# Kernel optimization log

Measured on AMD Instinct MI355X. Metric: run time of the kernel, lower is better.

Reference implementation:

```python
import jax, jax.numpy as jnp
import numpy as np

C = 256
K = 9
PAD = (K - 1) // 2  # 4


def setup_inputs() -> dict:
    key = jax.random.key(0)
    k1, k2, k3 = jax.random.split(key, 3)
    fea = jax.random.normal(k1, (8, C, 128, 128), dtype=jnp.float32)
    # Conv2d(C, C, (1,9)) with kernel height 1 -> 1D conv weight [O, I, K]
    fan_in = C * K
    bound = 1.0 / np.sqrt(fan_in)
    weight = jax.random.uniform(k2, (C, C, K), dtype=jnp.float32, minval=-bound, maxval=bound)
    bias = jax.random.uniform(k3, (C,), dtype=jnp.float32, minval=-bound, maxval=bound)
    return {"fea": fea, "weight": weight, "bias": bias}


def _conv_relu(x, weight, bias):
    # x: [n, c, w] -> 1D conv along width, then ReLU (matches Conv2d (1,9) on a 1-row slice)
    y = jax.lax.conv_general_dilated(
        x, weight, window_strides=(1,), padding=[(PAD, PAD)],
        dimension_numbers=("NCW", "OIW", "NCW"))
    return jax.nn.relu(y + bias[None, :, None])


def reference(fea, weight, bias):
    n, c, h, w = fea.shape
    rows = jnp.moveaxis(fea, 2, 0)  # [h, n, c, w]

    def step(carry, row):
        new = _conv_relu(carry, weight, bias) + row
        return new, new

    # forward (top-down) scan: fea_stack[i] = conv(fea_stack[i-1]) + fea_stack[i]
    _, ys_f = jax.lax.scan(step, rows[0], rows[1:])
    full = jnp.concatenate([rows[:1], ys_f], axis=0)  # [h, n, c, w]

    # backward (bottom-up) scan over i = h-2 .. 1
    mid = full[1:h - 1]
    _, ys_b = jax.lax.scan(step, full[h - 1], mid[::-1])
    out_rows = jnp.concatenate([full[:1], ys_b[::-1], full[h - 1:]], axis=0)

    return jnp.moveaxis(out_rows, 0, 2)  # back to [n, c, h, w]
```

## Files before the change

### kernel.cpp

```cpp
#include <hip/hip_runtime.h>

typedef _Float16 f16;
typedef _Float16 f16x8 __attribute__((ext_vector_type(8)));
typedef _Float16 f16x4 __attribute__((ext_vector_type(4)));
typedef float    f32x16 __attribute__((ext_vector_type(16)));
typedef unsigned long long u64;

#define N_   8
#define C_   256
#define H_   128
#define W_   128
#define K_   9
#define PAD_ 4
#define WP_  136

#define WELEMS (8*9*16*64*8)
#define XT_SZ  (N_*WP_*256)
#define XBUF_F16 (N_*WP_*512)
#define NBLK   256
#define NSTEP  253

__device__ __host__ inline int xpos(int ci, int wp) {
    int g = ((ci >> 3) + 2 * wp) & 31;
    return g * 8 + (ci & 7);
}

__global__ __launch_bounds__(256) void prep_w(const float* __restrict__ w,
                                              f16* __restrict__ wh, f16* __restrict__ wl) {
    int t = blockIdx.x * 256 + threadIdx.x;
    if (t >= WELEMS) return;
    int j = t & 7;      int q = t >> 3;
    int lane = q & 63;  q >>= 6;
    int c = q & 15;     q >>= 4;
    int k = q % 9;      int ct = q / 9;
    int co = ct * 32 + (lane & 31);
    int ci = c * 16 + (lane >> 5) * 8 + j;
    float wf = w[(co * C_ + ci) * K_ + k];
    f16 hi = (f16)wf;
    f16 lo = (f16)(wf - (float)hi);
    wh[t] = hi;  wl[t] = lo;
}

__global__ __launch_bounds__(256) void prep_x0(const float* __restrict__ fea,
                                               f16* __restrict__ xb0, f16* __restrict__ xb1) {
    int t = blockIdx.x * 256 + threadIdx.x;
    if (t >= XT_SZ) return;
    int ci = t & 255;
    int wp = (t >> 8) % WP_;
    int n  = t / (WP_ * 256);
    int w  = wp - PAD_;
    bool pad = (unsigned)w >= (unsigned)W_;
    float v = pad ? 0.0f : fea[((size_t)(n * C_ + ci) * H_ + 0) * W_ + w];
    f16 hi = (f16)v;
    f16 lo = (f16)(v - (float)hi);
    size_t row = ((size_t)n * WP_ + wp) * 512;
    int p = xpos(ci, wp);
    xb0[row + p] = hi;  xb0[row + 256 + p] = lo;
    if (pad) { xb1[row + p] = (f16)0.f; xb1[row + 256 + p] = (f16)0.f; }
}

__global__ __launch_bounds__(256) void copy_row0(const float* __restrict__ fea,
                                                 float* __restrict__ out) {
    int idx = blockIdx.x * 256 + threadIdx.x;
    if (idx >= N_ * C_ * W_) return;
    int w = idx % W_;
    int nc = idx / W_;
    size_t off = (size_t)nc * (H_ * W_) + w;
    out[off] = fea[off];
}

__global__ __launch_bounds__(512, 2) void conv_persist(
    f16* __restrict__ xb0, f16* __restrict__ xb1,
    const f16* __restrict__ whp, const f16* __restrict__ wlp,
    const float* __restrict__ bias, const float* __restrict__ fea,
    float* out, unsigned* ctr)
{
    __shared__ unsigned char Xs[40 * 1024];
    float* red = (float*)Xs;

    const int b   = blockIdx.x;
    const int n   = b & 7;
    const int ct  = (b >> 3) & 7;
    const int wq  = b >> 6;
    const int w0  = wq * 32;
    const int tid = threadIdx.x;
    const int wv  = tid >> 6;
    const int l   = tid & 63;
    const int m   = l & 31;
    const int hh  = l >> 5;
    unsigned* flags = ctr + n * 64;
    const int bslot = b >> 3;

    f16x8 wkh[9][2], wkl[9][2];
    #pragma unroll
    for (int k = 0; k < 9; ++k)
        #pragma unroll
        for (int cs = 0; cs < 2; ++cs) {
            size_t o = ((((size_t)ct * 9 + k) * 16 + (wv * 2 + cs)) * 64 + l) * 8;
            wkh[k][cs] = *(const f16x8*)&whp[o];
            wkl[k][cs] = *(const f16x8*)&wlp[o];
        }

    f16* bufs[2] = {xb0, xb1};

    const int dq = wv & 3;
    const int co_base = ct * 32 + dq * 8 + hh * 4;
    const size_t HW = (size_t)H_ * W_;
    float4 bv = *(const float4*)&bias[co_base];
    const float bvr[4] = {bv.x, bv.y, bv.z, bv.w};

    for (int step = 0; step < NSTEP; ++step) {
        const int  cur   = step & 1;
        const bool fwd   = step < 127;
        const int  h_out = fwd ? (step + 1) : (NSTEP - step);
        const float* radd = fwd ? fea : out;
        const size_t obase = (((size_t)(n * C_ + co_base)) * H_ + h_out) * W_ + w0 + m;

        {
            const u64* src = (const u64*)(bufs[cur] + ((size_t)n * WP_ + w0) * 512);
            u64 v[10];
            #pragma unroll
            for (int ii = 0; ii < 10; ++ii)
                v[ii] = __hip_atomic_load(src + ii * 512 + tid,
                                          __ATOMIC_RELAXED, __HIP_MEMORY_SCOPE_AGENT);
            #pragma unroll
            for (int ii = 0; ii < 10; ++ii)
                *(u64*)(Xs + (size_t)(ii * 512 + tid) * 8) = v[ii];
        }
        float rv[4] = {0.f, 0.f, 0.f, 0.f};
        if (wv < 4) {
            #pragma unroll
            for (int c2 = 0; c2 < 4; ++c2)
                rv[c2] = radd[obase + (size_t)c2 * HW];
        }
        __syncthreads();

        f32x16 a0{}, cr{};
        #pragma unroll
        for (int k = 0; k < 9; ++k) {
            #pragma unroll
            for (int cs = 0; cs < 2; ++cs) {
                const int rl  = m + k;
                const int gsw = (((wv * 2 + cs) * 2 + hh + 2 * rl) & 31) * 16;
                const unsigned char* base = Xs + rl * 1024 + gsw;
                f16x8 bh = *(const f16x8*)base;
                f16x8 bl = *(const f16x8*)(base + 512);
                a0 = __builtin_amdgcn_mfma_f32_32x32x16_f16(wkh[k][cs], bh, a0, 0, 0, 0);
                cr = __builtin_amdgcn_mfma_f32_32x32x16_f16(wkh[k][cs], bl, cr, 0, 0, 0);
                cr = __builtin_amdgcn_mfma_f32_32x32x16_f16(wkl[k][cs], bh, cr, 0, 0, 0);
            }
        }
        __syncthreads();

        {
            f32x16 sp = a0 + cr;
            #pragma unroll
            for (int reg = 0; reg < 16; ++reg)
                red[(reg * 8 + wv) * 64 + l] = sp[reg];
        }
        __syncthreads();

        if (wv < 4) {
            float y[4];
            #pragma unroll
            for (int c2 = 0; c2 < 4; ++c2) {
                const int reg = dq * 4 + c2;
                float s = 0.f;
                #pragma unroll
                for (int cc = 0; cc < 8; ++cc)
                    s += red[(reg * 8 + cc) * 64 + l];
                y[c2] = fmaxf(s + bvr[c2], 0.0f) + rv[c2];
                out[obase + (size_t)c2 * HW] = y[c2];
            }
            const int wp = w0 + m + PAD_;
            const size_t row = ((size_t)n * WP_ + wp) * 512;
            const int g   = (ct * 4 + dq + 2 * wp) & 31;
            const int pos = g * 8 + hh * 4;
            f16x4 hv, lv;
            #pragma unroll
            for (int c2 = 0; c2 < 4; ++c2) {
                f16 hi = (f16)y[c2];
                hv[c2] = hi;
                lv[c2] = (f16)(y[c2] - (float)hi);
            }
            u64 uh, ul;
            __builtin_memcpy(&uh, &hv, 8);
            __builtin_memcpy(&ul, &lv, 8);
            f16* xbn = bufs[cur ^ 1];
            __hip_atomic_store((u64*)&xbn[row + pos],       uh, __ATOMIC_RELAXED, __HIP_MEMORY_SCOPE_AGENT);
            __hip_atomic_store((u64*)&xbn[row + 256 + pos], ul, __ATOMIC_RELAXED, __HIP_MEMORY_SCOPE_AGENT);
        }

        if (step < NSTEP - 1) {
            asm volatile("s_waitcnt vmcnt(0)" ::: "memory");
            __syncthreads();
            const unsigned tgt = (unsigned)(step + 1);
            if (tid == 0)
                __hip_atomic_store(flags + bslot, tgt, __ATOMIC_RELAXED, __HIP_MEMORY_SCOPE_AGENT);
            if (wv == 0) {
                while (true) {
                    unsigned v = tgt;
                    if (l < 32)
                        v = __hip_atomic_load(flags + l, __ATOMIC_RELAXED, __HIP_MEMORY_SCOPE_AGENT);
                    if (__all((int)(v >= tgt))) break;
                    __builtin_amdgcn_s_sleep(1);
                }
            }
            __syncthreads();
        }
    }
}

__global__ __launch_bounds__(256) void step_f32(
    const float* __restrict__ xprev, const float* __restrict__ radd,
    float* __restrict__ yout, const float* __restrict__ wsrc,
    const float* __restrict__ bias, int h_prev, int h_out)
{
    __shared__ float XsF[C_][40];
    const int t  = threadIdx.x;
    const int bx = blockIdx.x;
    const int n  = bx & 7;
    const int wb = (bx >> 3) & 3;
    const int cb = bx >> 5;
    const int w0 = wb * 32;
    {
        const size_t nbase = (size_t)n * C_ * (H_ * W_) + (size_t)h_prev * W_;
        for (int idx = t; idx < C_ * 40; idx += 256) {
            int ci = idx / 40;
            int j  = idx - ci * 40;
            int w  = w0 - PAD_ + j;
            float v = 0.0f;
            if ((unsigned)w < (unsigned)W_)
                v = xprev[nbase + (size_t)ci * (H_ * W_) + w];
            XsF[ci][j] = v;
        }
    }
    __syncthreads();
    const int co = cb * 32 + (t >> 3);
    const int w4 = (t & 7) * 4;
    const float* wr = wsrc + (size_t)co * (C_ * K_);
    float acc0 = 0.f, acc1 = 0.f, acc2 = 0.f, acc3 = 0.f;
    for (int ci = 0; ci < C_; ci++) {
        float wk[K_];
        #pragma unroll
        for (int k = 0; k < K_; k++) wk[k] = wr[ci * K_ + k];
        float xv[12];
        float4 a = *(const float4*)&XsF[ci][w4];
        float4 bq = *(const float4*)&XsF[ci][w4 + 4];
        float4 c = *(const float4*)&XsF[ci][w4 + 8];
        xv[0]=a.x; xv[1]=a.y; xv[2]=a.z; xv[3]=a.w;
        xv[4]=bq.x; xv[5]=bq.y; xv[6]=bq.z; xv[7]=bq.w;
        xv[8]=c.x; xv[9]=c.y; xv[10]=c.z; xv[11]=c.w;
        #pragma unroll
        for (int k = 0; k < K_; k++) {
            acc0 = fmaf(wk[k], xv[k],     acc0);
            acc1 = fmaf(wk[k], xv[k + 1], acc1);
            acc2 = fmaf(wk[k], xv[k + 2], acc2);
            acc3 = fmaf(wk[k], xv[k + 3], acc3);
        }
    }
    const float bb = bias[co];
    const size_t obase = (((size_t)n * C_ + co) * H_ + h_out) * W_ + w0 + w4;
    float4 r = *(const float4*)&radd[obase];
    float4 o;
    o.x = fmaxf(acc0 + bb, 0.f) + r.x;
    o.y = fmaxf(acc1 + bb, 0.f) + r.y;
    o.z = fmaxf(acc2 + bb, 0.f) + r.z;
    o.w = fmaxf(acc3 + bb, 0.f) + r.w;
    *(float4*)&yout[obase] = o;
}

extern "C" void kernel_launch(void* const* d_in, const int* in_sizes, int n_in,
                              void* d_out, int out_size, void* d_ws, size_t ws_size,
                              hipStream_t stream) {
    const float* fea    = (const float*)d_in[0];
    const float* weight = (const float*)d_in[1];
    const float* bias   = (const float*)d_in[2];
    float* out = (float*)d_out;

    const size_t need = (size_t)2 * WELEMS * 2 + (size_t)2 * XBUF_F16 * 2 + 2048;

    copy_row0<<<(N_ * C_ * W_ + 255) / 256, 256, 0, stream>>>(fea, out);

    if (ws_size >= need && d_ws != nullptr) {
        f16* wh  = (f16*)d_ws;
        f16* wl  = wh + WELEMS;
        f16* xb0 = wl + WELEMS;
        f16* xb1 = xb0 + XBUF_F16;
        unsigned* ctr = (unsigned*)(xb1 + XBUF_F16);

        hipMemsetAsync(ctr, 0, 2048, stream);
        prep_w<<<(WELEMS + 255) / 256, 256, 0, stream>>>(weight, wh, wl);
        prep_x0<<<(XT_SZ + 255) / 256, 256, 0, stream>>>(fea, xb0, xb1);

        conv_persist<<<NBLK, 512, 0, stream>>>(xb0, xb1, wh, wl, bias, fea, out, ctr);
    } else {
        for (int h = 1; h < H_; h++)
            step_f32<<<256, 256, 0, stream>>>(out, fea, out, weight, bias, h - 1, h);
        for (int h = H_ - 2; h >= 1; h--)
            step_f32<<<256, 256, 0, stream>>>(out, out, out, weight, bias, h + 1, h);
    }
}
```

Baseline: 1.481 ms.

## Restructure per-step grid sync with LDS wave counter and separate reduce buffer

```diff
diff --git a/kernel.cpp b/kernel.cpp
--- a/kernel.cpp
+++ b/kernel.cpp
@@ -19,6 +19,7 @@
 #define XBUF_F16 (N_*WP_*512)
 #define NBLK   256
 #define NSTEP  253
+#define LDS_BYTES (40960 + 32768 + 128)
 
 __device__ __host__ inline int xpos(int ci, int wp) {
     int g = ((ci >> 3) + 2 * wp) & 31;
@@ -69,14 +70,17 @@
     out[off] = fea[off];
 }
 
-__global__ __launch_bounds__(512, 2) void conv_persist(
+__global__ __launch_bounds__(512)
+__attribute__((amdgpu_waves_per_eu(2, 2)))
+void conv_persist(
     f16* __restrict__ xb0, f16* __restrict__ xb1,
     const f16* __restrict__ whp, const f16* __restrict__ wlp,
     const float* __restrict__ bias, const float* __restrict__ fea,
     float* out, unsigned* ctr)
 {
-    __shared__ unsigned char Xs[40 * 1024];
-    float* red = (float*)Xs;
+    extern __shared__ unsigned char Xs[];
+    float*    red  = (float*)(Xs + 40960);
+    unsigned* wcnt = (unsigned*)(Xs + 40960 + 32768);
 
     const int b   = blockIdx.x;
     const int n   = b & 7;
@@ -91,6 +95,8 @@
     unsigned* flags = ctr + n * 64;
     const int bslot = b >> 3;
 
+    if (tid == 0) *wcnt = 0;
+
     f16x8 wkh[9][2], wkl[9][2];
     #pragma unroll
     for (int k = 0; k < 9; ++k)
@@ -100,6 +106,17 @@
             wkh[k][cs] = *(const f16x8*)&whp[o];
             wkl[k][cs] = *(const f16x8*)&wlp[o];
         }
+    {
+        f16 z0 = (f16)(0.0f * bias[0]);
+        #pragma unroll
+        for (int k = 0; k < 9; ++k)
+            #pragma unroll
+            for (int cs = 0; cs < 2; ++cs) {
+                #pragma unroll
+                for (int j = 0; j < 8; ++j) { wkh[k][cs][j] += z0; wkl[k][cs][j] += z0; }
+            }
+    }
+    __syncthreads();
 
     f16* bufs[2] = {xb0, xb1};
 
@@ -118,14 +135,21 @@
 
         {
             const u64* src = (const u64*)(bufs[cur] + ((size_t)n * WP_ + w0) * 512);
-            u64 v[10];
-            #pragma unroll
-            for (int ii = 0; ii < 10; ++ii)
-                v[ii] = __hip_atomic_load(src + ii * 512 + tid,
-                                          __ATOMIC_RELAXED, __HIP_MEMORY_SCOPE_AGENT);
-            #pragma unroll
-            for (int ii = 0; ii < 10; ++ii)
-                *(u64*)(Xs + (size_t)(ii * 512 + tid) * 8) = v[ii];
+            u64 va[5], vb[5];
+            #pragma unroll
+            for (int ii = 0; ii < 5; ++ii) {
+                int g = tid + ii * 512;
+                va[ii] = __hip_atomic_load(src + (size_t)g * 2,     __ATOMIC_RELAXED, __HIP_MEMORY_SCOPE_AGENT);
+                vb[ii] = __hip_atomic_load(src + (size_t)g * 2 + 1, __ATOMIC_RELAXED, __HIP_MEMORY_SCOPE_AGENT);
+            }
+            #pragma unroll
+            for (int ii = 0; ii < 5; ++ii) {
+                int g = tid + ii * 512;
+                u64 p[2] = {va[ii], vb[ii]};
+                uint4 qd;
+                __builtin_memcpy(&qd, p, 16);
+                *(uint4*)(Xs + (size_t)g * 16) = qd;
+            }
         }
         float rv[4] = {0.f, 0.f, 0.f, 0.f};
         if (wv < 4) {
@@ -150,7 +174,6 @@
                 cr = __builtin_amdgcn_mfma_f32_32x32x16_f16(wkl[k][cs], bh, cr, 0, 0, 0);
             }
         }
-        __syncthreads();
 
         {
             f32x16 sp = a0 + cr;
@@ -170,44 +193,51 @@
                 for (int cc = 0; cc < 8; ++cc)
                     s += red[(reg * 8 + cc) * 64 + l];
                 y[c2] = fmaxf(s + bvr[c2], 0.0f) + rv[c2];
-                out[obase + (size_t)c2 * HW] = y[c2];
-            }
-            const int wp = w0 + m + PAD_;
-            const size_t row = ((size_t)n * WP_ + wp) * 512;
-            const int g   = (ct * 4 + dq + 2 * wp) & 31;
-            const int pos = g * 8 + hh * 4;
-            f16x4 hv, lv;
-            #pragma unroll
-            for (int c2 = 0; c2 < 4; ++c2) {
-                f16 hi = (f16)y[c2];
-                hv[c2] = hi;
-                lv[c2] = (f16)(y[c2] - (float)hi);
-            }
-            u64 uh, ul;
-            __builtin_memcpy(&uh, &hv, 8);
-            __builtin_memcpy(&ul, &lv, 8);
-            f16* xbn = bufs[cur ^ 1];
-            __hip_atomic_store((u64*)&xbn[row + pos],       uh, __ATOMIC_RELAXED, __HIP_MEMORY_SCOPE_AGENT);
-            __hip_atomic_store((u64*)&xbn[row + 256 + pos], ul, __ATOMIC_RELAXED, __HIP_MEMORY_SCOPE_AGENT);
-        }
-
-        if (step < NSTEP - 1) {
-            asm volatile("s_waitcnt vmcnt(0)" ::: "memory");
-            __syncthreads();
-            const unsigned tgt = (unsigned)(step + 1);
-            if (tid == 0)
-                __hip_atomic_store(flags + bslot, tgt, __ATOMIC_RELAXED, __HIP_MEMORY_SCOPE_AGENT);
-            if (wv == 0) {
-                while (true) {
-                    unsigned v = tgt;
-                    if (l < 32)
-                        v = __hip_atomic_load(flags + l, __ATOMIC_RELAXED, __HIP_MEMORY_SCOPE_AGENT);
-                    if (__all((int)(v >= tgt))) break;
-                    __builtin_amdgcn_s_sleep(1);
+            }
+            if (step < NSTEP - 1) {
+                const int wp = w0 + m + PAD_;
+                const size_t row = ((size_t)n * WP_ + wp) * 512;
+                const int g   = (ct * 4 + dq + 2 * wp) & 31;
+                const int pos = g * 8 + hh * 4;
+                f16x4 hv, lv;
+                #pragma unroll
+                for (int c2 = 0; c2 < 4; ++c2) {
+                    f16 hi = (f16)y[c2];
+                    hv[c2] = hi;
+                    lv[c2] = (f16)(y[c2] - (float)hi);
                 }
-            }
-            __syncthreads();
-        }
+                u64 uh, ul;
+                __builtin_memcpy(&uh, &hv, 8);
+                __builtin_memcpy(&ul, &lv, 8);
+                f16* xbn = bufs[cur ^ 1];
+                __hip_atomic_store((u64*)&xbn[row + pos],       uh, __ATOMIC_RELAXED, __HIP_MEMORY_SCOPE_AGENT);
+                __hip_atomic_store((u64*)&xbn[row + 256 + pos], ul, __ATOMIC_RELAXED, __HIP_MEMORY_SCOPE_AGENT);
+                asm volatile("s_waitcnt vmcnt(0)" ::: "memory");
+                if (l == 0)
+                    __hip_atomic_fetch_add(wcnt, 1u, __ATOMIC_RELAXED, __HIP_MEMORY_SCOPE_WORKGROUP);
+                const unsigned tgt = (unsigned)(step + 1);
+                if (wv == 0 && l == 0) {
+                    while (__hip_atomic_load(wcnt, __ATOMIC_RELAXED, __HIP_MEMORY_SCOPE_WORKGROUP) < 4u * tgt) {}
+                    __hip_atomic_store(flags + bslot, tgt, __ATOMIC_RELAXED, __HIP_MEMORY_SCOPE_AGENT);
+                }
+                #pragma unroll
+                for (int c2 = 0; c2 < 4; ++c2)
+                    out[obase + (size_t)c2 * HW] = y[c2];
+                if (wv == 0) {
+                    while (true) {
+                        unsigned v = tgt;
+                        if (l < 32)
+                            v = __hip_atomic_load(flags + l, __ATOMIC_RELAXED, __HIP_MEMORY_SCOPE_AGENT);
+                        if (__all((int)(v >= tgt))) break;
+                    }
+                }
+            } else {
+                #pragma unroll
+                for (int c2 = 0; c2 < 4; ++c2)
+                    out[obase + (size_t)c2 * HW] = y[c2];
+            }
+        }
+        __syncthreads();
     }
 }
 
@@ -293,7 +323,9 @@
         prep_w<<<(WELEMS + 255) / 256, 256, 0, stream>>>(weight, wh, wl);
         prep_x0<<<(XT_SZ + 255) / 256, 256, 0, stream>>>(fea, xb0, xb1);
 
-        conv_persist<<<NBLK, 512, 0, stream>>>(xb0, xb1, wh, wl, bias, fea, out, ctr);
+        hipFuncSetAttribute((const void*)conv_persist,
+                            hipFuncAttributeMaxDynamicSharedMemorySize, LDS_BYTES);
+        conv_persist<<<NBLK, 512, LDS_BYTES, stream>>>(xb0, xb1, wh, wl, bias, fea, out, ctr);
     } else {
         for (int h = 1; h < H_; h++)
             step_f32<<<256, 256, 0, stream>>>(out, fea, out, weight, bias, h - 1, h);
```

After: 1.390 ms. 6.1% less time.
